# Kernel tuning notes

Hardware: AMD Instinct MI355X
Metric: run time of the kernel (lower is better)

Reference implementation:

```python
import jax, jax.numpy as jnp
import numpy as np

EPS = 1e-5  # torch BatchNorm1d default eps


def _bn(x, p):
    # eval-mode batchnorm; p = stacked [gamma, beta, running_mean, running_var], shape [4, C]
    g, b, m, v = p
    return (x - m[:, None]) * jax.lax.rsqrt(v[:, None] + EPS) * g[:, None] + b[:, None]


def _conv(w, x):
    # 1x1 Conv1d == channel matmul: w [O,C], x [B,C,N] -> [B,O,N]
    return jnp.einsum('oc,bcn->bon', w, x)


def _sa(x, qk_w, v_w, v_b, t_w, t_b, bnp):
    # offset self-attention; q_conv.weight is tied to k_conv.weight in the original
    q = jnp.einsum('oc,bcn->bno', qk_w, x)          # [B,N,C/4]
    k = _conv(qk_w, x)                              # [B,C/4,N]
    v = _conv(v_w, x) + v_b[None, :, None]          # [B,C,N]
    attn = jax.nn.softmax(jnp.einsum('bno,bom->bnm', q, k), axis=-1)  # [B,N,N]
    attn = attn / (1e-9 + attn.sum(axis=1, keepdims=True))            # L1 re-norm over dim 1
    x_r = jnp.einsum('bcn,bnm->bcm', v, attn)       # [B,C,N]
    x_r = jax.nn.relu(_bn(_conv(t_w, x - x_r) + t_b[None, :, None], bnp))
    return x + x_r


def setup_inputs():
    key = jax.random.key(0)
    ks = iter(jax.random.split(key, 64))
    def n(shape, s=0.1):
        return jax.random.normal(next(ks), shape, jnp.float32) * s
    def bn_p(c):
        g = jax.random.uniform(next(ks), (c,), jnp.float32, 0.5, 1.5)
        b = n((c,))
        m = n((c,))
        v = jax.random.uniform(next(ks), (c,), jnp.float32, 0.5, 1.5)
        return jnp.stack([g, b, m, v])
    B, C, N = 16, 16, 2048
    return {
        'x': jax.random.normal(next(ks), (B, C, N), jnp.float32),
        'conv1_w': n((128, 16)), 'bn1': bn_p(128),
        'conv2_w': n((16, 128)), 'bn2': bn_p(16),
        'sa_qk_w': n((4, 4, 16)), 'sa_v_w': n((4, 16, 16)), 'sa_v_b': n((4, 16)),
        'sa_trans_w': n((4, 16, 16)), 'sa_trans_b': n((4, 16)),
        'sa_bn': jnp.stack([bn_p(16) for _ in range(4)]),
        'fuse_w': n((128, 64)), 'fuse_bn': bn_p(128),
        'convs1_w': n((512, 264)), 'convs1_b': n((512,)), 'bns1': bn_p(512),
        'convs2_w': n((256, 512)), 'convs2_b': n((256,)), 'bns2': bn_p(256),
        'convs3_w': n((16, 256)), 'convs3_b': n((16,)),
    }


def reference(x, conv1_w, bn1, conv2_w, bn2, sa_qk_w, sa_v_w, sa_v_b,
              sa_trans_w, sa_trans_b, sa_bn, fuse_w, fuse_bn,
              convs1_w, convs1_b, bns1, convs2_w, convs2_b, bns2,
              convs3_w, convs3_b):
    B, _, N = x.shape
    h = jax.nn.relu(_bn(_conv(conv1_w, x), bn1))   # [B,128,N]
    h = jax.nn.relu(_bn(_conv(conv2_w, h), bn2))   # [B,16,N]
    feats = []
    for i in range(4):
        h = _sa(h, sa_qk_w[i], sa_v_w[i], sa_v_b[i], sa_trans_w[i], sa_trans_b[i], sa_bn[i])
        feats.append(h)
    xqq = jnp.concatenate(feats, axis=1)           # [B,64,N]
    xqqw = jax.nn.leaky_relu(_bn(_conv(fuse_w, xqq), fuse_bn), 0.2)  # [B,128,N]
    # faithful to original (including the [1]-indexing quirk):
    x_max = jnp.argmax(xqqw, axis=2)               # [B,128] argmax indices (torch.max(...)[1])
    x_avg = jnp.mean(xqqw, axis=2)[1]              # [128] batch element 1's channel means
    x_max_f = jnp.broadcast_to(x_max.astype(jnp.float32)[:, :, None], (B, 128, N))
    x_avg_f = jnp.broadcast_to(x_avg.reshape(B, -1)[:, :, None], (B, 128 // B, N))
    g = jnp.concatenate([xqqw, x_max_f, x_avg_f], axis=1)  # [B,264,N]
    g = jax.nn.relu(_bn(_conv(convs1_w, g) + convs1_b[None, :, None], bns1))
    # dropout is identity in eval mode
    g = jax.nn.relu(_bn(_conv(convs2_w, g) + convs2_b[None, :, None], bns2))
    return _conv(convs3_w, g) + convs3_b[None, :, None]  # [B,16,N]
```

## Files before the change

### kernel.cpp

```cpp
#include <hip/hip_runtime.h>
#include <stdint.h>

typedef __bf16 bf16_t;
typedef __bf16 bf16x8 __attribute__((ext_vector_type(8)));
typedef __bf16 bf16x4 __attribute__((ext_vector_type(4)));
typedef float f32x4 __attribute__((ext_vector_type(4)));
typedef float f32x2 __attribute__((ext_vector_type(2)));

#define LOG2E 1.4426950408889634f

__device__ __forceinline__ float relu_(float v) { return v > 0.f ? v : 0.f; }

__global__ __launch_bounds__(256) void k_prep(
    const float* __restrict__ convs1_w, const float* __restrict__ convs2_w,
    const float* __restrict__ bn1, const float* __restrict__ bn2,
    const float* __restrict__ sa_bn, const float* __restrict__ sa_trans_b,
    const float* __restrict__ fuse_bn, const float* __restrict__ convs1_b,
    const float* __restrict__ bns1, const float* __restrict__ convs2_b,
    const float* __restrict__ bns2,
    bf16_t* __restrict__ wbuf1, bf16_t* __restrict__ wbuf2, float* __restrict__ params)
{
  int idx = blockIdx.x * 256 + threadIdx.x;
  for (int it = 0; it < 3; ++it) {
    int i = idx + it * 65536;
    if (i < 65536) {
      int o = i >> 7, c = i & 127;
      wbuf1[i] = (bf16_t)convs1_w[o * 264 + c];
    } else if (i < 65536 + 131072) {
      int j = i - 65536;
      wbuf2[j] = (bf16_t)convs2_w[j];
    }
  }
  if (blockIdx.x == 0) {
    for (int t = threadIdx.x; t < 1104; t += 256) {
      float g, be, m, v, extra = 0.f; int so, ho;
      if (t < 128)      { g=bn1[t]; be=bn1[128+t]; m=bn1[256+t]; v=bn1[384+t]; so=t; ho=128+t; }
      else if (t < 144) { int u=t-128; g=bn2[u]; be=bn2[16+u]; m=bn2[32+u]; v=bn2[48+u]; so=256+u; ho=272+u; }
      else if (t < 208) { int u=t-144; int L=u>>4, o=u&15; const float* p=sa_bn+L*64;
                          g=p[o]; be=p[16+o]; m=p[32+o]; v=p[48+o];
                          extra=sa_trans_b[L*16+o]; so=288+u; ho=352+u; }
      else if (t < 336) { int u=t-208; g=fuse_bn[u]; be=fuse_bn[128+u]; m=fuse_bn[256+u]; v=fuse_bn[384+u]; so=416+u; ho=544+u; }
      else if (t < 848) { int u=t-336; g=bns1[u]; be=bns1[512+u]; m=bns1[1024+u]; v=bns1[1536+u]; extra=convs1_b[u]; so=672+u; ho=1184+u; }
      else              { int u=t-848; g=bns2[u]; be=bns2[256+u]; m=bns2[512+u]; v=bns2[768+u]; extra=convs2_b[u]; so=1696+u; ho=1952+u; }
      float sc = g * rsqrtf(v + 1e-5f);
      params[so] = sc;
      params[ho] = (extra - m) * sc + be;
    }
  }
}

__global__ __launch_bounds__(256) void k_convs(const float* __restrict__ x,
    const float* __restrict__ w1, const float* __restrict__ w2,
    const float* __restrict__ params, const float* __restrict__ qk_w,
    const float* __restrict__ v_w, const float* __restrict__ v_b,
    float* __restrict__ h0, float* __restrict__ kbuf, float* __restrict__ vbuf)
{
  __shared__ __align__(16) float xs[16 * 128];
  __shared__ float ws1[128 * 17];
  __shared__ float ws2[16 * 129];
  __shared__ __align__(16) float h1s[128 * 64];
  __shared__ float hcv[128 * 17];
  __shared__ float qk[64], vw[256], vb[16], sc1[128], sh1[128], sc2[16], sh2[16];
  int t = threadIdx.x;
  int bid = blockIdx.x;
  int b = bid >> 4, n0 = (bid & 15) * 128;
  for (int i = t; i < 2048; i += 256) { int c = i >> 7, col = i & 127; xs[c * 128 + col] = x[((size_t)b * 16 + c) * 2048 + n0 + col]; }
  for (int i = t; i < 2048; i += 256) { int o = i >> 4, c = i & 15;  ws1[o * 17 + c]  = w1[i]; }
  for (int i = t; i < 2048; i += 256) { int o = i >> 7, c = i & 127; ws2[o * 129 + c] = w2[i]; }
  if (t < 64) qk[t] = qk_w[t];
  vw[t] = v_w[t];
  if (t < 16) { vb[t] = v_b[t]; sc2[t] = params[256 + t]; sh2[t] = params[272 + t]; }
  if (t < 128) { sc1[t] = params[t]; sh1[t] = params[128 + t]; }
  __syncthreads();
  int colh = t & 63, hi4 = t >> 6;
  int cg = t & 15, og = t >> 4;
  for (int h = 0; h < 2; ++h) {
    int cb = h * 64;
    float xr[16];
#pragma unroll
    for (int c = 0; c < 16; ++c) xr[c] = xs[c * 128 + cb + colh];
#pragma unroll 4
    for (int i = 0; i < 32; ++i) {
      int o = (i << 2) | hi4;
      float s = 0.f;
#pragma unroll
      for (int c = 0; c < 16; ++c) s = fmaf(ws1[o * 17 + c], xr[c], s);
      h1s[o * 64 + colh] = relu_(fmaf(s, sc1[o], sh1[o]));
    }
    __syncthreads();
    float a0 = 0.f, a1 = 0.f, a2 = 0.f, a3 = 0.f;
    for (int c = 0; c < 128; ++c) {
      float4 f = *(const float4*)&h1s[c * 64 + cg * 4];
      float w = ws2[og * 129 + c];
      a0 = fmaf(w, f.x, a0); a1 = fmaf(w, f.y, a1);
      a2 = fmaf(w, f.z, a2); a3 = fmaf(w, f.w, a3);
    }
    float4 v4;
    v4.x = relu_(fmaf(a0, sc2[og], sh2[og]));
    v4.y = relu_(fmaf(a1, sc2[og], sh2[og]));
    v4.z = relu_(fmaf(a2, sc2[og], sh2[og]));
    v4.w = relu_(fmaf(a3, sc2[og], sh2[og]));
    *(float4*)&h0[((size_t)b * 16 + og) * 2048 + n0 + cb + cg * 4] = v4;
    hcv[(cb + cg * 4 + 0) * 17 + og] = v4.x;
    hcv[(cb + cg * 4 + 1) * 17 + og] = v4.y;
    hcv[(cb + cg * 4 + 2) * 17 + og] = v4.z;
    hcv[(cb + cg * 4 + 3) * 17 + og] = v4.w;
    __syncthreads();
  }
  int col = t & 127, ug = t >> 7;
  float hr[16];
#pragma unroll
  for (int c = 0; c < 16; ++c) hr[c] = hcv[col * 17 + c];
#pragma unroll
  for (int i = 0; i < 10; ++i) {
    int u = ug * 10 + i;
    const float* W = (u < 4) ? &qk[u * 16] : &vw[(u - 4) * 16];
    float s = (u < 4) ? 0.f : vb[u - 4];
#pragma unroll
    for (int c = 0; c < 16; ++c) s = fmaf(W[c], hr[c], s);
    if (u < 4) kbuf[((size_t)b * 2048 + n0 + col) * 4 + u] = s;
    else       vbuf[((size_t)b * 16 + (u - 4)) * 2048 + n0 + col] = s;
  }
}

__global__ __launch_bounds__(256) void k_rowstats(const float* __restrict__ kbuf, float* __restrict__ Lpart)
{
  __shared__ float4 kch[256];
  int bid = blockIdx.x;
  int b = bid >> 6, nt = (bid >> 3) & 7, ms = bid & 7;
  int t = threadIdx.x;
  const float4* kb = (const float4*)kbuf + b * 2048;
  kch[t] = kb[ms * 256 + t];
  __syncthreads();
  int n = nt * 256 + t;
  float4 q = kb[n];
  q.x *= LOG2E; q.y *= LOG2E; q.z *= LOG2E; q.w *= LOG2E;
  float L = 0.f;
#pragma unroll 4
  for (int m = 0; m < 256; ++m) {
    float4 k4 = kch[m];
    float s = fmaf(q.x, k4.x, fmaf(q.y, k4.y, fmaf(q.z, k4.z, q.w * k4.w)));
    L += exp2f(s);
  }
  Lpart[((size_t)ms * 16 + b) * 2048 + n] = L;
}

__global__ __launch_bounds__(256) void k_colaccum(const float* __restrict__ kbuf, const float* __restrict__ vbuf,
    const float* __restrict__ Lpart, float* __restrict__ parts)
{
  __shared__ __align__(16) float ku[512 * 8];
  __shared__ __align__(16) float vch[512 * 16];
  int bid = blockIdx.x;
  int b = bid >> 5, mt = (bid >> 2) & 7, ns = bid & 3;
  int t = threadIdx.x;
  int m = mt * 256 + t;
  float4 q = ((const float4*)kbuf)[b * 2048 + m];
  f32x2 q01 = {q.x * LOG2E, q.y * LOG2E};
  f32x2 q23 = {q.z * LOG2E, q.w * LOG2E};
  for (int i = t; i < 512; i += 256) {
    int n = ns * 512 + i;
    float4 kk = ((const float4*)kbuf)[b * 2048 + n];
    float Ls = 0.f;
#pragma unroll
    for (int s = 0; s < 8; ++s) Ls += Lpart[((size_t)s * 16 + b) * 2048 + n];
    *(float4*)&ku[i * 8] = kk;
    ku[i * 8 + 4] = 1.0f / Ls;
#pragma unroll
    for (int c = 0; c < 16; ++c) vch[i * 16 + c] = vbuf[((size_t)b * 16 + c) * 2048 + n];
  }
  __syncthreads();
  f32x2 acc[8];
#pragma unroll
  for (int j = 0; j < 8; ++j) acc[j] = (f32x2){0.f, 0.f};
  float den = 0.f;
#pragma unroll 2
  for (int nn = 0; nn < 512; ++nn) {
    const f32x2* kp = (const f32x2*)&ku[nn * 8];
    f32x2 p = q01 * kp[0];
    p = q23 * kp[1] + p;
    float s = p[0] + p[1];
    float e = exp2f(s) * ku[nn * 8 + 4];
    den += e;
    f32x2 ev = {e, e};
    const f32x2* vp = (const f32x2*)&vch[nn * 16];
    acc[0] += ev * vp[0]; acc[1] += ev * vp[1];
    acc[2] += ev * vp[2]; acc[3] += ev * vp[3];
    acc[4] += ev * vp[4]; acc[5] += ev * vp[5];
    acc[6] += ev * vp[6]; acc[7] += ev * vp[7];
  }
  float* p = parts + ((size_t)(ns * 16 + b) * 17) * 2048 + m;
#pragma unroll
  for (int c = 0; c < 16; ++c) p[(size_t)c * 2048] = acc[c >> 1][c & 1];
  p[(size_t)16 * 2048] = den;
}

__global__ __launch_bounds__(256) void k_epilogue(const float* __restrict__ parts,
    const float* __restrict__ hin, int hbs, const float* __restrict__ t_w,
    const float* __restrict__ params, int layer, float* __restrict__ hout,
    const float* __restrict__ qk_w, const float* __restrict__ v_w, const float* __restrict__ v_b,
    float* __restrict__ kbuf, float* __restrict__ vbuf)
{
  __shared__ float pd[17 * 64];
  __shared__ float hs[16 * 64];
  __shared__ float dl[16 * 64];
  __shared__ float hv[64 * 17];
  __shared__ float tw[256], qk[64], vw[256], vb[16], sc[16], sh[16];
  int t = threadIdx.x;
  int bid = blockIdx.x;
  int b = bid >> 5, n0 = (bid & 31) * 64;
  tw[t] = t_w[t];
  if (qk_w) { if (t < 64) qk[t] = qk_w[t]; vw[t] = v_w[t]; if (t < 16) vb[t] = v_b[t]; }
  if (t < 16) { sc[t] = params[288 + layer * 16 + t]; sh[t] = params[352 + layer * 16 + t]; }
  for (int i = t; i < 1088; i += 256) {
    int r = i >> 6, c = i & 63;
    float s = 0.f;
#pragma unroll
    for (int sp = 0; sp < 4; ++sp)
      s += parts[((size_t)(sp * 16 + b) * 17 + r) * 2048 + n0 + c];
    pd[i] = s;
  }
  for (int i = t; i < 1024; i += 256) {
    int c = i >> 6, col = i & 63;
    hs[i] = hin[(size_t)b * hbs + (size_t)c * 2048 + n0 + col];
  }
  __syncthreads();
  int col = t & 63, g4 = t >> 6;
  float inv = 1.f / (1e-9f + pd[16 * 64 + col]);
#pragma unroll
  for (int j = 0; j < 4; ++j) {
    int c = g4 * 4 + j;
    dl[c * 64 + col] = hs[c * 64 + col] - pd[c * 64 + col] * inv;
  }
  __syncthreads();
#pragma unroll
  for (int j = 0; j < 4; ++j) {
    int o = g4 * 4 + j;
    float y = 0.f;
#pragma unroll
    for (int c = 0; c < 16; ++c) y = fmaf(tw[o * 16 + c], dl[c * 64 + col], y);
    y = relu_(fmaf(y, sc[o], sh[o]));
    float hh = hs[o * 64 + col] + y;
    hout[(size_t)b * 64 * 2048 + (size_t)o * 2048 + n0 + col] = hh;
    hv[col * 17 + o] = hh;
  }
  if (qk_w) {
    __syncthreads();
    float hr[16];
#pragma unroll
    for (int c = 0; c < 16; ++c) hr[c] = hv[col * 17 + c];
#pragma unroll
    for (int i = 0; i < 5; ++i) {
      int u = g4 * 5 + i;
      const float* W = (u < 4) ? &qk[u * 16] : &vw[(u - 4) * 16];
      float s = (u < 4) ? 0.f : vb[u - 4];
#pragma unroll
      for (int c = 0; c < 16; ++c) s = fmaf(W[c], hr[c], s);
      if (u < 4) kbuf[((size_t)b * 2048 + n0 + col) * 4 + u] = s;
      else       vbuf[((size_t)b * 16 + (u - 4)) * 2048 + n0 + col] = s;
    }
  }
}

__global__ __launch_bounds__(256) void k_fuse(const float* __restrict__ feats, const float* __restrict__ fw,
    const float* __restrict__ params, float* __restrict__ xqqw, bf16_t* __restrict__ gbuf)
{
  __shared__ float ws[128 * 65];
  __shared__ __align__(16) float fst[64 * 64];
  __shared__ float sc[128], sh[128];
  int t = threadIdx.x, bid = blockIdx.x;
  int b = bid >> 5, n0 = (bid & 31) * 64;
  for (int i = t; i < 8192; i += 256) { int o = i >> 6, c = i & 63; ws[o * 65 + c] = fw[i]; }
  for (int i = t; i < 4096; i += 256) { int c = i >> 6, col = i & 63; fst[i] = feats[((size_t)b * 64 + c) * 2048 + n0 + col]; }
  if (t < 128) { sc[t] = params[416 + t]; sh[t] = params[544 + t]; }
  __syncthreads();
  int cg = t & 7, og = t >> 3;
  f32x2 acc[4][4];
#pragma unroll
  for (int oo = 0; oo < 4; ++oo)
#pragma unroll
    for (int j = 0; j < 4; ++j) acc[oo][j] = (f32x2){0.f, 0.f};
  for (int c = 0; c < 64; ++c) {
    const f32x2* fp = (const f32x2*)&fst[c * 64 + cg * 8];
    f32x2 f0 = fp[0], f1 = fp[1], f2v = fp[2], f3 = fp[3];
#pragma unroll
    for (int oo = 0; oo < 4; ++oo) {
      float w = ws[(og * 4 + oo) * 65 + c];
      f32x2 wv = {w, w};
      acc[oo][0] += wv * f0; acc[oo][1] += wv * f1;
      acc[oo][2] += wv * f2v; acc[oo][3] += wv * f3;
    }
  }
  float y[4][8];
#pragma unroll
  for (int oo = 0; oo < 4; ++oo) {
    int o = og * 4 + oo;
    float s0 = sc[o], s1 = sh[o];
#pragma unroll
    for (int j = 0; j < 8; ++j) {
      float v = fmaf(acc[oo][j >> 1][j & 1], s0, s1);
      y[oo][j] = v > 0.f ? v : 0.2f * v;
    }
    float4 v0 = {y[oo][0], y[oo][1], y[oo][2], y[oo][3]};
    float4 v1 = {y[oo][4], y[oo][5], y[oo][6], y[oo][7]};
    *(float4*)&xqqw[((size_t)b * 128 + o) * 2048 + n0 + cg * 8] = v0;
    *(float4*)&xqqw[((size_t)b * 128 + o) * 2048 + n0 + cg * 8 + 4] = v1;
  }
#pragma unroll
  for (int j = 0; j < 8; ++j) {
    int col = n0 + cg * 8 + j;
    bf16x4 pk;
    pk[0] = (bf16_t)y[0][j]; pk[1] = (bf16_t)y[1][j];
    pk[2] = (bf16_t)y[2][j]; pk[3] = (bf16_t)y[3][j];
    *(bf16x4*)&gbuf[((size_t)b * 2048 + col) * 128 + og * 4] = pk;
  }
}

__global__ __launch_bounds__(256) void k_argmax(const float* __restrict__ xqqw,
    float* __restrict__ xmaxf, float* __restrict__ xavg)
{
  __shared__ float sv[256]; __shared__ int si[256]; __shared__ float ss[256];
  int bo = blockIdx.x;
  int b = bo >> 7, o = bo & 127;
  const float* row = xqqw + (size_t)bo * 2048;
  int tid = threadIdx.x;
  float best = -3.4e38f; int bi = 0; float sum = 0.f;
#pragma unroll
  for (int j = 0; j < 8; ++j) {
    int n = j * 256 + tid;
    float v = row[n];
    sum += v;
    if (v > best) { best = v; bi = n; }
  }
  sv[tid] = best; si[tid] = bi; ss[tid] = sum;
  __syncthreads();
  for (int s = 128; s > 0; s >>= 1) {
    if (tid < s) {
      float v2 = sv[tid + s]; int i2 = si[tid + s];
      if (v2 > sv[tid] || (v2 == sv[tid] && i2 < si[tid])) { sv[tid] = v2; si[tid] = i2; }
      ss[tid] += ss[tid + s];
    }
    __syncthreads();
  }
  if (tid == 0) {
    xmaxf[bo] = (float)si[0];
    if (b == 1) xavg[o] = ss[0] * (1.0f / 2048.0f);
  }
}

__global__ __launch_bounds__(256) void k_bias2(const float* __restrict__ w1,
    const float* __restrict__ xmaxf, const float* __restrict__ xavg,
    const float* __restrict__ params, float* __restrict__ bias2)
{
  int id = blockIdx.x * 256 + threadIdx.x;
  int o = id >> 4, b = id & 15;
  const float* wr = w1 + (size_t)o * 264;
  float s = 0.f;
  for (int u = 0; u < 128; ++u) s = fmaf(wr[128 + u], xmaxf[b * 128 + u], s);
#pragma unroll
  for (int u = 0; u < 8; ++u)  s = fmaf(wr[256 + u], xavg[b * 8 + u], s);
  bias2[b * 512 + o] = s * params[672 + o];
}

__global__ __launch_bounds__(256) void k_gemm(const bf16_t* __restrict__ A, const bf16_t* __restrict__ Bm,
    const float* __restrict__ scp, const float* __restrict__ shp, const float* __restrict__ bias2,
    bf16_t* __restrict__ Cout, int M, int K, int mtiles)
{
  __shared__ bf16_t At[128 * 32];
  __shared__ bf16_t Bt[128 * 32];
  int tid = threadIdx.x;
  int mt = blockIdx.x % mtiles, ct = blockIdx.x / mtiles;
  int srow = tid >> 2, scol = (tid & 3) << 3;
  const bf16_t* ga = A  + (size_t)(mt * 128 + srow) * K + scol;
  const bf16_t* gb = Bm + (size_t)(ct * 128 + srow) * K + scol;
  int lane = tid & 63, wave = tid >> 6;
  int wr = (wave >> 1) * 64, wc = (wave & 1) * 64;
  int frow = lane & 15, fk = (lane >> 4) * 8;
  const f32x4 z4 = {0.f, 0.f, 0.f, 0.f};
  f32x4 acc[4][4];
#pragma unroll
  for (int i = 0; i < 4; ++i)
#pragma unroll
    for (int j = 0; j < 4; ++j) acc[i][j] = z4;
  uint4 ra0 = *(const uint4*)ga, ra1 = *(const uint4*)(ga + (size_t)64 * K);
  uint4 rb0 = *(const uint4*)gb, rb1 = *(const uint4*)(gb + (size_t)64 * K);
  int ksteps = K >> 5;
  for (int ks = 0; ks < ksteps; ++ks) {
    __syncthreads();
    *(uint4*)&At[tid * 8] = ra0;  *(uint4*)&At[2048 + tid * 8] = ra1;
    *(uint4*)&Bt[tid * 8] = rb0;  *(uint4*)&Bt[2048 + tid * 8] = rb1;
    __syncthreads();
    if (ks + 1 < ksteps) {
      ra0 = *(const uint4*)(ga + (ks + 1) * 32);
      ra1 = *(const uint4*)(ga + (size_t)64 * K + (ks + 1) * 32);
      rb0 = *(const uint4*)(gb + (ks + 1) * 32);
      rb1 = *(const uint4*)(gb + (size_t)64 * K + (ks + 1) * 32);
    }
    bf16x8 af[4], bfr[4];
#pragma unroll
    for (int i = 0; i < 4; ++i) af[i]  = *(const bf16x8*)&At[(wr + i * 16 + frow) * 32 + fk];
#pragma unroll
    for (int j = 0; j < 4; ++j) bfr[j] = *(const bf16x8*)&Bt[(wc + j * 16 + frow) * 32 + fk];
#pragma unroll
    for (int i = 0; i < 4; ++i)
#pragma unroll
      for (int j = 0; j < 4; ++j)
        acc[i][j] = __builtin_amdgcn_mfma_f32_16x16x32_bf16(af[i], bfr[j], acc[i][j], 0, 0, 0);
  }
  int crow = (lane >> 4) * 4, ccol = lane & 15;
#pragma unroll
  for (int i = 0; i < 4; ++i) {
    int o0 = mt * 128 + wr + i * 16 + crow;
    float s0 = scp[o0], s1 = scp[o0+1], s2 = scp[o0+2], s3 = scp[o0+3];
    float t0 = shp[o0], t1 = shp[o0+1], t2 = shp[o0+2], t3 = shp[o0+3];
#pragma unroll
    for (int j = 0; j < 4; ++j) {
      int bn = ct * 128 + wc + j * 16 + ccol;
      float b0 = 0.f, b1 = 0.f, b2 = 0.f, b3 = 0.f;
      if (bias2) {
        const float* bp = bias2 + (size_t)(bn >> 11) * M + o0;
        b0 = bp[0]; b1 = bp[1]; b2 = bp[2]; b3 = bp[3];
      }
      bf16x4 pk;
      pk[0] = (bf16_t)relu_(fmaf(acc[i][j][0], s0, t0 + b0));
      pk[1] = (bf16_t)relu_(fmaf(acc[i][j][1], s1, t1 + b1));
      pk[2] = (bf16_t)relu_(fmaf(acc[i][j][2], s2, t2 + b2));
      pk[3] = (bf16_t)relu_(fmaf(acc[i][j][3], s3, t3 + b3));
      *(bf16x4*)(Cout + (size_t)bn * M + o0) = pk;
    }
  }
}

__global__ __launch_bounds__(128) void k_gemm3(const bf16_t* __restrict__ g2, const float* __restrict__ w3,
    const float* __restrict__ b3, float* __restrict__ out)
{
  __shared__ float wsT[4096];
  __shared__ float bb[16];
  int tid = threadIdx.x;
  for (int i = tid; i < 4096; i += 128) { int o = i >> 8, k = i & 255; wsT[k * 16 + o] = w3[i]; }
  if (tid < 16) bb[tid] = b3[tid];
  __syncthreads();
  int col = blockIdx.x * 128 + tid;
  int b = col >> 11, n = col & 2047;
  const bf16_t* g = g2 + (size_t)col * 256;
  float acc[16];
#pragma unroll
  for (int o = 0; o < 16; ++o) acc[o] = 0.f;
  for (int k0 = 0; k0 < 256; k0 += 8) {
    bf16x8 gv8 = *(const bf16x8*)(g + k0);
#pragma unroll
    for (int kk = 0; kk < 8; ++kk) {
      float gv = (float)gv8[kk];
      const float* wr = &wsT[(k0 + kk) * 16];
#pragma unroll
      for (int o = 0; o < 16; ++o) acc[o] = fmaf(wr[o], gv, acc[o]);
    }
  }
  float* op = out + (size_t)b * 16 * 2048 + n;
#pragma unroll
  for (int o = 0; o < 16; ++o) op[(size_t)o * 2048] = acc[o] + bb[o];
}

extern "C" void kernel_launch(void* const* d_in, const int* in_sizes, int n_in,
                              void* d_out, int out_size, void* d_ws, size_t ws_size,
                              hipStream_t stream)
{
  const float* x         = (const float*)d_in[0];
  const float* conv1_w   = (const float*)d_in[1];
  const float* bn1       = (const float*)d_in[2];
  const float* conv2_w   = (const float*)d_in[3];
  const float* bn2       = (const float*)d_in[4];
  const float* sa_qk_w   = (const float*)d_in[5];
  const float* sa_v_w    = (const float*)d_in[6];
  const float* sa_v_b    = (const float*)d_in[7];
  const float* sa_trans_w= (const float*)d_in[8];
  const float* sa_trans_b= (const float*)d_in[9];
  const float* sa_bn     = (const float*)d_in[10];
  const float* fuse_w    = (const float*)d_in[11];
  const float* fuse_bn   = (const float*)d_in[12];
  const float* convs1_w  = (const float*)d_in[13];
  const float* convs1_b  = (const float*)d_in[14];
  const float* bns1      = (const float*)d_in[15];
  const float* convs2_w  = (const float*)d_in[16];
  const float* convs2_b  = (const float*)d_in[17];
  const float* bns2      = (const float*)d_in[18];
  const float* convs3_w  = (const float*)d_in[19];
  const float* convs3_b  = (const float*)d_in[20];

  char* ws = (char*)d_ws;
  float*  xqqw  = (float*)(ws + 0);
  float*  feats = (float*)(ws + 16777216);
  float*  h0    = (float*)(ws + 25165824);
  float*  kbuf  = (float*)(ws + 27262976);
  float*  vbuf  = (float*)(ws + 27787264);
  float*  Lpart = (float*)(ws + 29884416);
  float*  parts = (float*)(ws + 31981568);
  bf16_t* gbuf  = (bf16_t*)(ws + 42991616);
  bf16_t* g2    = (bf16_t*)(ws + 51380224);
  bf16_t* g1    = (bf16_t*)(ws + 0);
  bf16_t* wbuf1 = (bf16_t*)(ws + 68157440);
  bf16_t* wbuf2 = (bf16_t*)(ws + 68288512);
  float*  params= (float*)(ws + 68550656);
  float*  xmaxf = (float*)(ws + 68567040);
  float*  xavg  = (float*)(ws + 68575232);
  float*  bias2 = (float*)(ws + 68579328);

  k_prep<<<256, 256, 0, stream>>>(convs1_w, convs2_w, bn1, bn2, sa_bn, sa_trans_b, fuse_bn,
                                  convs1_b, bns1, convs2_b, bns2, wbuf1, wbuf2, params);
  k_convs<<<256, 256, 0, stream>>>(x, conv1_w, conv2_w, params, sa_qk_w, sa_v_w, sa_v_b,
                                   h0, kbuf, vbuf);
  for (int i = 0; i < 4; ++i) {
    k_rowstats<<<1024, 256, 0, stream>>>(kbuf, Lpart);
    k_colaccum<<<512, 256, 0, stream>>>(kbuf, vbuf, Lpart, parts);
    const float* hin = (i == 0) ? h0 : (feats + (size_t)(i - 1) * 16 * 2048);
    int hbs = (i == 0) ? 16 * 2048 : 64 * 2048;
    bool last = (i == 3);
    k_epilogue<<<512, 256, 0, stream>>>(parts, hin, hbs, sa_trans_w + i * 256, params, i,
        feats + (size_t)i * 16 * 2048,
        last ? nullptr : sa_qk_w + (i + 1) * 64,
        last ? nullptr : sa_v_w + (i + 1) * 256,
        last ? nullptr : sa_v_b + (i + 1) * 16,
        kbuf, vbuf);
  }
  k_fuse<<<512, 256, 0, stream>>>(feats, fuse_w, params, xqqw, gbuf);
  k_argmax<<<2048, 256, 0, stream>>>(xqqw, xmaxf, xavg);
  k_bias2<<<32, 256, 0, stream>>>(convs1_w, xmaxf, xavg, params, bias2);
  k_gemm<<<1024, 256, 0, stream>>>(wbuf1, gbuf, params + 672, params + 1184, bias2, g1, 512, 128, 4);
  k_gemm<<<512, 256, 0, stream>>>(wbuf2, g1, params + 1696, params + 1952, nullptr, g2, 256, 512, 2);
  k_gemm3<<<256, 128, 0, stream>>>(g2, convs3_w, convs3_b, (float*)d_out);
}
```

Measured before the change: 564.4 us.

## Register-block two query columns per thread in colaccum and transpose V layout

k_colaccum now handles two m columns per thread over a 256-wide n chunk, so each LDS load of k and v feeds two exp/accumulate chains, and the n split grows from 4 to 8. The 1/L row normaliser is folded into the exponent as -log2(L), which removes a multiply per element. V is stored position-major (vbufT) so the chunk load uses float4 reads. The cost is more partial buffers for the epilogue to reduce (8 instead of 4), more registers per thread, and a shifted workspace layout.

```diff
diff --git a/kernel.cpp b/kernel.cpp
--- a/kernel.cpp
+++ b/kernel.cpp
@@ -53,7 +53,7 @@
     const float* __restrict__ w1, const float* __restrict__ w2,
     const float* __restrict__ params, const float* __restrict__ qk_w,
     const float* __restrict__ v_w, const float* __restrict__ v_b,
-    float* __restrict__ h0, float* __restrict__ kbuf, float* __restrict__ vbuf)
+    float* __restrict__ h0, float* __restrict__ kbuf, float* __restrict__ vbufT)
 {
   __shared__ __align__(16) float xs[16 * 128];
   __shared__ float ws1[128 * 17];
@@ -119,7 +119,7 @@
 #pragma unroll
     for (int c = 0; c < 16; ++c) s = fmaf(W[c], hr[c], s);
     if (u < 4) kbuf[((size_t)b * 2048 + n0 + col) * 4 + u] = s;
-    else       vbuf[((size_t)b * 16 + (u - 4)) * 2048 + n0 + col] = s;
+    else       vbufT[((size_t)b * 2048 + n0 + col) * 16 + (u - 4)] = s;
   }
 }
 
@@ -145,60 +145,66 @@
   Lpart[((size_t)ms * 16 + b) * 2048 + n] = L;
 }
 
-__global__ __launch_bounds__(256) void k_colaccum(const float* __restrict__ kbuf, const float* __restrict__ vbuf,
+__global__ __launch_bounds__(256) void k_colaccum(const float* __restrict__ kbuf, const float* __restrict__ vbufT,
     const float* __restrict__ Lpart, float* __restrict__ parts)
 {
-  __shared__ __align__(16) float ku[512 * 8];
-  __shared__ __align__(16) float vch[512 * 16];
+  __shared__ __align__(16) float ku[256 * 8];
+  __shared__ __align__(16) float vch[256 * 16];
   int bid = blockIdx.x;
-  int b = bid >> 5, mt = (bid >> 2) & 7, ns = bid & 3;
+  int b = bid >> 5, mt = (bid >> 3) & 3, ns = bid & 7;
   int t = threadIdx.x;
-  int m = mt * 256 + t;
-  float4 q = ((const float4*)kbuf)[b * 2048 + m];
-  f32x2 q01 = {q.x * LOG2E, q.y * LOG2E};
-  f32x2 q23 = {q.z * LOG2E, q.w * LOG2E};
-  for (int i = t; i < 512; i += 256) {
-    int n = ns * 512 + i;
-    float4 kk = ((const float4*)kbuf)[b * 2048 + n];
+  {
+    int n = ns * 256 + t;
+    float4 k4 = ((const float4*)kbuf)[b * 2048 + n];
     float Ls = 0.f;
 #pragma unroll
     for (int s = 0; s < 8; ++s) Ls += Lpart[((size_t)s * 16 + b) * 2048 + n];
-    *(float4*)&ku[i * 8] = kk;
-    ku[i * 8 + 4] = 1.0f / Ls;
-#pragma unroll
-    for (int c = 0; c < 16; ++c) vch[i * 16 + c] = vbuf[((size_t)b * 16 + c) * 2048 + n];
-  }
-  __syncthreads();
-  f32x2 acc[8];
-#pragma unroll
-  for (int j = 0; j < 8; ++j) acc[j] = (f32x2){0.f, 0.f};
-  float den = 0.f;
+    *(float4*)&ku[t * 8] = k4;
+    ku[t * 8 + 4] = -__log2f(Ls);
+    const float4* vp = (const float4*)&vbufT[((size_t)b * 2048 + n) * 16];
+    *(float4*)&vch[t * 16 + 0]  = vp[0];
+    *(float4*)&vch[t * 16 + 4]  = vp[1];
+    *(float4*)&vch[t * 16 + 8]  = vp[2];
+    *(float4*)&vch[t * 16 + 12] = vp[3];
+  }
+  __syncthreads();
+  int m0 = mt * 512 + t;
+  float4 qa = ((const float4*)kbuf)[b * 2048 + m0];
+  float4 qb = ((const float4*)kbuf)[b * 2048 + m0 + 256];
+  qa.x *= LOG2E; qa.y *= LOG2E; qa.z *= LOG2E; qa.w *= LOG2E;
+  qb.x *= LOG2E; qb.y *= LOG2E; qb.z *= LOG2E; qb.w *= LOG2E;
+  f32x2 acc0[8], acc1[8];
+#pragma unroll
+  for (int j = 0; j < 8; ++j) { acc0[j] = (f32x2){0.f, 0.f}; acc1[j] = (f32x2){0.f, 0.f}; }
+  float den0 = 0.f, den1 = 0.f;
 #pragma unroll 2
-  for (int nn = 0; nn < 512; ++nn) {
-    const f32x2* kp = (const f32x2*)&ku[nn * 8];
-    f32x2 p = q01 * kp[0];
-    p = q23 * kp[1] + p;
-    float s = p[0] + p[1];
-    float e = exp2f(s) * ku[nn * 8 + 4];
-    den += e;
-    f32x2 ev = {e, e};
+  for (int nn = 0; nn < 256; ++nn) {
+    f32x4 k4 = *(const f32x4*)&ku[nn * 8];
+    float lg = ku[nn * 8 + 4];
+    float s0 = fmaf(qa.x, k4[0], fmaf(qa.y, k4[1], fmaf(qa.z, k4[2], fmaf(qa.w, k4[3], lg))));
+    float s1 = fmaf(qb.x, k4[0], fmaf(qb.y, k4[1], fmaf(qb.z, k4[2], fmaf(qb.w, k4[3], lg))));
+    float e0 = exp2f(s0), e1 = exp2f(s1);
+    den0 += e0; den1 += e1;
+    f32x2 ev0 = {e0, e0}, ev1 = {e1, e1};
     const f32x2* vp = (const f32x2*)&vch[nn * 16];
-    acc[0] += ev * vp[0]; acc[1] += ev * vp[1];
-    acc[2] += ev * vp[2]; acc[3] += ev * vp[3];
-    acc[4] += ev * vp[4]; acc[5] += ev * vp[5];
-    acc[6] += ev * vp[6]; acc[7] += ev * vp[7];
-  }
-  float* p = parts + ((size_t)(ns * 16 + b) * 17) * 2048 + m;
-#pragma unroll
-  for (int c = 0; c < 16; ++c) p[(size_t)c * 2048] = acc[c >> 1][c & 1];
-  p[(size_t)16 * 2048] = den;
+#pragma unroll
+    for (int j = 0; j < 8; ++j) { f32x2 v2 = vp[j]; acc0[j] += ev0 * v2; acc1[j] += ev1 * v2; }
+  }
+  float* p = parts + ((size_t)(ns * 16 + b) * 17) * 2048 + m0;
+#pragma unroll
+  for (int c = 0; c < 16; ++c) p[(size_t)c * 2048] = acc0[c >> 1][c & 1];
+  p[(size_t)16 * 2048] = den0;
+  p += 256;
+#pragma unroll
+  for (int c = 0; c < 16; ++c) p[(size_t)c * 2048] = acc1[c >> 1][c & 1];
+  p[(size_t)16 * 2048] = den1;
 }
 
 __global__ __launch_bounds__(256) void k_epilogue(const float* __restrict__ parts,
     const float* __restrict__ hin, int hbs, const float* __restrict__ t_w,
     const float* __restrict__ params, int layer, float* __restrict__ hout,
     const float* __restrict__ qk_w, const float* __restrict__ v_w, const float* __restrict__ v_b,
-    float* __restrict__ kbuf, float* __restrict__ vbuf)
+    float* __restrict__ kbuf, float* __restrict__ vbufT)
 {
   __shared__ float pd[17 * 64];
   __shared__ float hs[16 * 64];
@@ -215,7 +221,7 @@
     int r = i >> 6, c = i & 63;
     float s = 0.f;
 #pragma unroll
-    for (int sp = 0; sp < 4; ++sp)
+    for (int sp = 0; sp < 8; ++sp)
       s += parts[((size_t)(sp * 16 + b) * 17 + r) * 2048 + n0 + c];
     pd[i] = s;
   }
@@ -256,7 +262,7 @@
 #pragma unroll
       for (int c = 0; c < 16; ++c) s = fmaf(W[c], hr[c], s);
       if (u < 4) kbuf[((size_t)b * 2048 + n0 + col) * 4 + u] = s;
-      else       vbuf[((size_t)b * 16 + (u - 4)) * 2048 + n0 + col] = s;
+      else       vbufT[((size_t)b * 2048 + n0 + col) * 16 + (u - 4)] = s;
     }
   }
 }
@@ -491,26 +497,26 @@
   float*  feats = (float*)(ws + 16777216);
   float*  h0    = (float*)(ws + 25165824);
   float*  kbuf  = (float*)(ws + 27262976);
-  float*  vbuf  = (float*)(ws + 27787264);
+  float*  vbufT = (float*)(ws + 27787264);
   float*  Lpart = (float*)(ws + 29884416);
-  float*  parts = (float*)(ws + 31981568);
-  bf16_t* gbuf  = (bf16_t*)(ws + 42991616);
-  bf16_t* g2    = (bf16_t*)(ws + 51380224);
+  float*  parts = (float*)(ws + 30932992);
+  bf16_t* gbuf  = (bf16_t*)(ws + 48758784);
+  bf16_t* g2    = (bf16_t*)(ws + 57147392);
   bf16_t* g1    = (bf16_t*)(ws + 0);
-  bf16_t* wbuf1 = (bf16_t*)(ws + 68157440);
-  bf16_t* wbuf2 = (bf16_t*)(ws + 68288512);
-  float*  params= (float*)(ws + 68550656);
-  float*  xmaxf = (float*)(ws + 68567040);
-  float*  xavg  = (float*)(ws + 68575232);
-  float*  bias2 = (float*)(ws + 68579328);
+  bf16_t* wbuf1 = (bf16_t*)(ws + 73924608);
+  bf16_t* wbuf2 = (bf16_t*)(ws + 74055680);
+  float*  params= (float*)(ws + 74317824);
+  float*  xmaxf = (float*)(ws + 74334208);
+  float*  xavg  = (float*)(ws + 74342400);
+  float*  bias2 = (float*)(ws + 74346496);
 
   k_prep<<<256, 256, 0, stream>>>(convs1_w, convs2_w, bn1, bn2, sa_bn, sa_trans_b, fuse_bn,
                                   convs1_b, bns1, convs2_b, bns2, wbuf1, wbuf2, params);
   k_convs<<<256, 256, 0, stream>>>(x, conv1_w, conv2_w, params, sa_qk_w, sa_v_w, sa_v_b,
-                                   h0, kbuf, vbuf);
+                                   h0, kbuf, vbufT);
   for (int i = 0; i < 4; ++i) {
     k_rowstats<<<1024, 256, 0, stream>>>(kbuf, Lpart);
-    k_colaccum<<<512, 256, 0, stream>>>(kbuf, vbuf, Lpart, parts);
+    k_colaccum<<<512, 256, 0, stream>>>(kbuf, vbufT, Lpart, parts);
     const float* hin = (i == 0) ? h0 : (feats + (size_t)(i - 1) * 16 * 2048);
     int hbs = (i == 0) ? 16 * 2048 : 64 * 2048;
     bool last = (i == 3);
@@ -519,7 +525,7 @@
         last ? nullptr : sa_qk_w + (i + 1) * 64,
         last ? nullptr : sa_v_w + (i + 1) * 256,
         last ? nullptr : sa_v_b + (i + 1) * 16,
-        kbuf, vbuf);
+        kbuf, vbufT);
   }
   k_fuse<<<512, 256, 0, stream>>>(feats, fuse_w, params, xqqw, gbuf);
   k_argmax<<<2048, 256, 0, stream>>>(xqqw, xmaxf, xavg);
```

Measured after the change: 551.9 us. 2.2% less time.
